# Performance work log

Measured on AMD Instinct MI355X. Metric: run time of the kernel, lower is better.

## Reference

```python
import jax, jax.numpy as jnp
import numpy as np

# Model dims (match init_kwargs / input_specs)
B, CIN, COUT = 32, 32, 64
H, W = 128, 128
KH, KW = 3, 3
MAXCN = 64                    # max entries in connect_nums_list
HO, WO = H - KH + 1, W - KW + 1   # padding=0, stride=1


def setup_inputs() -> dict:
    key = jax.random.key(0)
    k1, k2, k3, k4 = jax.random.split(key, 4)
    x = jax.random.normal(k1, (B, CIN, H, W), dtype=jnp.float32)
    # padded kernel bank: [out_channel, connection_slot, kh, kw]
    weights = jax.random.normal(k2, (COUT, MAXCN, KH, KW), dtype=jnp.float32)
    # per-pixel bias map per output channel (original inits zeros; random exercises it)
    bias = jax.random.normal(k3, (COUT, HO, WO), dtype=jnp.float32) * 0.1
    connect_nums = jax.random.randint(k4, (COUT,), 1, MAXCN + 1, dtype=jnp.int32)
    return {"x": x, "weights": weights, "bias": bias, "connect_nums": connect_nums}


def reference(x, weights, bias, connect_nums):
    O, J = weights.shape[0], weights.shape[1]
    # mask out kernel slots beyond each channel's connection count
    mask = (jnp.arange(J)[None, :] < connect_nums[:, None]).astype(weights.dtype)  # [O,J]
    # slot j reads input channel j % CIN; conv is linear, so fold duplicate-channel
    # kernels into one effective dense kernel [O, CIN, KH, KW]
    onehot = jax.nn.one_hot(jnp.arange(J) % CIN, CIN, dtype=weights.dtype)  # [J,C]
    kdense = jnp.einsum('ojhw,oj,jc->ochw', weights, mask, onehot)
    out = jax.lax.conv_general_dilated(
        x, kdense, window_strides=(1, 1), padding='VALID',
        dimension_numbers=('NCHW', 'OIHW', 'NCHW'))  # [B,O,HO,WO]
    return out + bias[None]
```

## Files before the change

kernel.cpp:

```cpp
#include <hip/hip_runtime.h>

#define B_    32
#define CIN   32
#define COUT  64
#define H_    128
#define W_    128
#define HO_   126
#define WO_   126
#define MAXCN 64

typedef __attribute__((ext_vector_type(8))) short short8;
typedef __attribute__((ext_vector_type(4))) float floatx4;

static __device__ __forceinline__ unsigned short f2bf(float f) {
    union { float f; unsigned u; } v; v.f = f;
    unsigned r = v.u + 0x7fff + ((v.u >> 16) & 1);
    return (unsigned short)(r >> 16);
}

__global__ void fold_bf16(const float* __restrict__ w,
                          const int* __restrict__ cn,
                          unsigned short* __restrict__ wk) {
    int idx = blockIdx.x * 256 + threadIdx.x;
    if (idx >= 9 * COUT * CIN) return;
    int c   = idx & 31;
    int oc  = (idx >> 5) & 63;
    int tap = idx >> 11;
    int n = cn[oc];
    float v = 0.0f;
    if (c < n)      v += w[(oc * MAXCN + c) * 9 + tap];
    if (c + 32 < n) v += w[(oc * MAXCN + c + 32) * 9 + tap];
    wk[idx] = f2bf(v);
}

__global__ __launch_bounds__(256)
void nchw_to_nhwc_bf16(const float* __restrict__ x,
                       unsigned short* __restrict__ xb) {
    const int b = blockIdx.y, y = blockIdx.x;
    const int t = threadIdx.x;
    const int c8  = t & 3;
    const int xi0 = t >> 2;
    const float* xp = x + (size_t)b * CIN * H_ * W_ + (size_t)y * W_;
#pragma unroll
    for (int it = 0; it < 2; ++it) {
        const int xi = xi0 + it * 64;
        __align__(16) unsigned short v[8];
#pragma unroll
        for (int j = 0; j < 8; ++j) {
            const int c = c8 * 8 + j;
            v[j] = f2bf(xp[(size_t)c * (H_ * W_) + xi]);
        }
        *(uint4*)(xb + (((size_t)b * H_ + y) * W_ + xi) * CIN + c8 * 8) =
            *(const uint4*)v;
    }
}

__global__ __launch_bounds__(256, 4)
void conv_mfma(const unsigned short* __restrict__ xb,
               const unsigned short* __restrict__ wk,
               const float* __restrict__ bias,
               float* __restrict__ out) {
    __shared__ __align__(16) unsigned short ws[9 * COUT * CIN];

    const int tile = blockIdx.x;
    const int b    = blockIdx.y;
    const int tx = tile & 7, ty = tile >> 3;
    const int x0 = tx * 16, y0 = ty * 16;
    const int tid = threadIdx.x;

    uint4* ws4 = (uint4*)ws;
    const uint4* wk4 = (const uint4*)wk;
#pragma unroll
    for (int it = 0; it < 9; ++it) ws4[it * 256 + tid] = wk4[it * 256 + tid];
    __syncthreads();

    const int w_id = tid >> 6;
    const int lane = tid & 63;
    const int quad = lane >> 4, l16 = lane & 15;

    int rowoff[6];
#pragma unroll
    for (int r = 0; r < 6; ++r) {
        int iy = y0 + 4 * w_id + r; if (iy > H_ - 1) iy = H_ - 1;
        rowoff[r] = (b * H_ + iy) * (W_ * CIN);
    }
    int coloff[3];
#pragma unroll
    for (int kw = 0; kw < 3; ++kw) {
        int ix = x0 + l16 + kw; if (ix > W_ - 1) ix = W_ - 1;
        coloff[kw] = ix * CIN + quad * 8;
    }

    floatx4 acc[4][4];
#pragma unroll
    for (int i = 0; i < 4; ++i)
#pragma unroll
        for (int t = 0; t < 4; ++t) acc[i][t] = (floatx4)0.0f;

#pragma unroll
    for (int kh = 0; kh < 3; ++kh) {
#pragma unroll
        for (int kw = 0; kw < 3; ++kw) {
            const int tap = kh * 3 + kw;
            short8 a[4], bf[4];
#pragma unroll
            for (int t = 0; t < 4; ++t)
                a[t] = *(const short8*)&ws[((tap * COUT + t * 16 + l16) * CIN) + quad * 8];
#pragma unroll
            for (int i = 0; i < 4; ++i)
                bf[i] = *(const short8*)(xb + rowoff[i + kh] + coloff[kw]);
#pragma unroll
            for (int i = 0; i < 4; ++i)
#pragma unroll
                for (int t = 0; t < 4; ++t)
                    acc[i][t] = __builtin_amdgcn_mfma_f32_16x16x32_bf16(a[t], bf[i], acc[i][t], 0, 0, 0);
        }
    }

    const int col = x0 + l16;
    if (col < WO_) {
#pragma unroll
        for (int i = 0; i < 4; ++i) {
            const int y = y0 + 4 * w_id + i;
            if (y >= HO_) continue;
#pragma unroll
            for (int t = 0; t < 4; ++t) {
#pragma unroll
                for (int r = 0; r < 4; ++r) {
                    const int oc = t * 16 + quad * 4 + r;
                    out[(((size_t)b * COUT + oc) * HO_ + y) * WO_ + col] =
                        acc[i][t][r] + bias[((size_t)oc * HO_ + y) * WO_ + col];
                }
            }
        }
    }
}

__global__ void fold_kernel(const float* __restrict__ w,
                            const int* __restrict__ cn,
                            float* __restrict__ kd) {
    int idx = blockIdx.x * blockDim.x + threadIdx.x;
    if (idx >= COUT * CIN * 9) return;
    int t = idx % 9;
    int c = (idx / 9) % CIN;
    int o = idx / (9 * CIN);
    int n = cn[o];
    float v = 0.0f;
    if (c < n)      v += w[(o * MAXCN + c) * 9 + t];
    if (c + 32 < n) v += w[(o * MAXCN + c + 32) * 9 + t];
    kd[idx] = v;
}

__global__ __launch_bounds__(256)
void conv_kernel(const float* __restrict__ x,
                 const float* __restrict__ kd,
                 const float* __restrict__ bias,
                 float* __restrict__ out) {
    __shared__ __align__(16) float xsh[CIN * 18 * 20];
    __shared__ __align__(16) float wsh[16 * 289];
    const int b = blockIdx.z, ocg = blockIdx.y, tile = blockIdx.x;
    const int ty = tile >> 3, txx = tile & 7;
    const int y0 = ty * 16, x0 = txx * 16;
    const int tid = threadIdx.x;
    const float* xbp = x + (size_t)b * CIN * H_ * W_;
    for (int idx = tid; idx < CIN * 18 * 18; idx += 256) {
        int c = idx / 324, rem = idx - c * 324, r = rem / 18, col = rem - r * 18;
        int iy = y0 + r;   if (iy > H_ - 1) iy = H_ - 1;
        int ix = x0 + col; if (ix > W_ - 1) ix = W_ - 1;
        xsh[c * 360 + r * 20 + col] = xbp[(c * H_ + iy) * W_ + ix];
    }
    for (int idx = tid; idx < 16 * 288; idx += 256) {
        int oc = idx / 288, rr = idx - oc * 288;
        wsh[oc * 289 + rr] = kd[(ocg * 16 + oc) * 288 + rr];
    }
    __syncthreads();
    const int oc_l = tid & 15, pb = tid >> 4, pby = pb >> 2, pbx = pb & 3;
    float acc[4][4];
#pragma unroll
    for (int i = 0; i < 4; ++i)
#pragma unroll
        for (int j = 0; j < 4; ++j) acc[i][j] = 0.0f;
    const float* xp = &xsh[(pby * 4) * 20 + pbx * 4];
    const float* wp = &wsh[oc_l * 289];
    for (int c = 0; c < CIN; ++c) {
        float xr[6][6];
#pragma unroll
        for (int r = 0; r < 6; ++r) {
            const float* row = xp + c * 360 + r * 20;
            float4 v4 = *reinterpret_cast<const float4*>(row);
            float2 v2 = *reinterpret_cast<const float2*>(row + 4);
            xr[r][0] = v4.x; xr[r][1] = v4.y; xr[r][2] = v4.z;
            xr[r][3] = v4.w; xr[r][4] = v2.x; xr[r][5] = v2.y;
        }
        float wr[9];
#pragma unroll
        for (int t = 0; t < 9; ++t) wr[t] = wp[c * 9 + t];
#pragma unroll
        for (int kh = 0; kh < 3; ++kh)
#pragma unroll
            for (int kw = 0; kw < 3; ++kw) {
                const float wv = wr[kh * 3 + kw];
#pragma unroll
                for (int i = 0; i < 4; ++i)
#pragma unroll
                    for (int j = 0; j < 4; ++j)
                        acc[i][j] = fmaf(xr[i + kh][j + kw], wv, acc[i][j]);
            }
    }
    const int o = ocg * 16 + oc_l;
    const int yb = y0 + pby * 4, xq0 = x0 + pbx * 4;
    float* ob = out + ((size_t)(b * COUT + o)) * HO_ * WO_;
    const float* bb = bias + (size_t)o * HO_ * WO_;
#pragma unroll
    for (int i = 0; i < 4; ++i) {
        int y = yb + i;
        if (y >= HO_) continue;
#pragma unroll
        for (int j = 0; j < 4; ++j) {
            int xq = xq0 + j;
            if (xq >= WO_) continue;
            ob[y * WO_ + xq] = acc[i][j] + bb[y * WO_ + xq];
        }
    }
}

extern "C" void kernel_launch(void* const* d_in, const int* in_sizes, int n_in,
                              void* d_out, int out_size, void* d_ws, size_t ws_size,
                              hipStream_t stream) {
    const float* x    = (const float*)d_in[0];
    const float* w    = (const float*)d_in[1];
    const float* bias = (const float*)d_in[2];
    const int*   cn   = (const int*)d_in[3];
    float* out = (float*)d_out;

    const size_t XB_BYTES = (size_t)B_ * H_ * W_ * CIN * 2;
    const size_t WK_BYTES = (size_t)9 * COUT * CIN * 2;

    if (ws_size >= XB_BYTES + WK_BYTES) {
        unsigned short* xbuf = (unsigned short*)d_ws;
        unsigned short* wkb  = (unsigned short*)((char*)d_ws + XB_BYTES);
        fold_bf16<<<(9 * COUT * CIN + 255) / 256, 256, 0, stream>>>(w, cn, wkb);
        nchw_to_nhwc_bf16<<<dim3(H_, B_), 256, 0, stream>>>(x, xbuf);
        conv_mfma<<<dim3(64, B_), 256, 0, stream>>>(xbuf, wkb, bias, out);
    } else {
        float* kd = (float*)d_ws;
        fold_kernel<<<(COUT * CIN * 9 + 255) / 256, 256, 0, stream>>>(w, cn, kd);
        dim3 grid(64, 4, B_);
        conv_kernel<<<grid, 256, 0, stream>>>(x, kd, bias, out);
    }
}
```

Before: 281.8 us.

## Stage input tiles in LDS with double-buffered async loads across four column tiles

The MFMA conv kernel now handles four 16x16 output tiles per block. Each 18x18x32 bf16 input patch is staged into LDS with global_load_lds, double-buffered so the next tile's load overlaps the current tile's MFMAs, and the folded weights are stored in a chunked layout so LDS reads index cleanly. Bias is pre-transposed to an NHWC buffer by an extra kernel so the epilogue can read it with float4 loads. This removes repeated global loads of overlapping input pixels and amortizes the weight load over more tiles. In exchange the grid is smaller (512 blocks), LDS use is higher, and an extra bias-transpose pass and workspace are added.

```diff
diff --git a/kernel.cpp b/kernel.cpp
--- a/kernel.cpp
+++ b/kernel.cpp
@@ -16,6 +16,12 @@
     union { float f; unsigned u; } v; v.f = f;
     unsigned r = v.u + 0x7fff + ((v.u >> 16) & 1);
     return (unsigned short)(r >> 16);
+}
+
+static __device__ __forceinline__ void gld16(const void* g, void* l) {
+    __builtin_amdgcn_global_load_lds(
+        (const __attribute__((address_space(1))) unsigned int*)g,
+        (__attribute__((address_space(3))) unsigned int*)l, 16, 0, 0);
 }
 
 __global__ void fold_bf16(const float* __restrict__ w,
@@ -30,7 +36,7 @@
     float v = 0.0f;
     if (c < n)      v += w[(oc * MAXCN + c) * 9 + tap];
     if (c + 32 < n) v += w[(oc * MAXCN + c + 32) * 9 + tap];
-    wk[idx] = f2bf(v);
+    wk[((tap * 4 + (c >> 3)) * 64 + oc) * 8 + (c & 7)] = f2bf(v);
 }
 
 __global__ __launch_bounds__(256)
@@ -55,84 +61,124 @@
     }
 }
 
-__global__ __launch_bounds__(256, 4)
+__global__ __launch_bounds__(256)
+void bias_to_nhwc(const float* __restrict__ bias, float* __restrict__ bn) {
+    int idx = blockIdx.x * 256 + threadIdx.x;
+    int oc = idx & 63;
+    int p  = idx >> 6;
+    int y  = p / WO_;
+    int x  = p - y * WO_;
+    bn[idx] = bias[((size_t)oc * HO_ + y) * WO_ + x];
+}
+
+static __device__ __forceinline__
+void stage_tile(const unsigned short* __restrict__ xbi,
+                unsigned short* __restrict__ lds,
+                int w_id, int lane, int y0, int x0, int bsel) {
+    unsigned short* dst = lds + bsel * (1296 * 8);
+#pragma unroll
+    for (int k = 0; k < 5; ++k) {
+        const int base = w_id * 324 + k * 64;
+        const int d = base + lane;
+        const int q = d / 18, xc = d - q * 18;
+        const int row = q >> 2, cp = q & 3;
+        int iy = y0 + row; if (iy > H_ - 1) iy = H_ - 1;
+        int ix = x0 + xc;  if (ix > W_ - 1) ix = W_ - 1;
+        gld16(xbi + (((iy << 7) + ix) * 4 + cp) * 8, dst + base * 8);
+    }
+    {
+        const int base = w_id * 324 + 320;
+        if (lane < 4) {
+            const int d = base + lane;
+            const int q = d / 18, xc = d - q * 18;
+            const int row = q >> 2, cp = q & 3;
+            int iy = y0 + row; if (iy > H_ - 1) iy = H_ - 1;
+            int ix = x0 + xc;  if (ix > W_ - 1) ix = W_ - 1;
+            gld16(xbi + (((iy << 7) + ix) * 4 + cp) * 8, dst + base * 8);
+        }
+    }
+}
+
+__global__ __launch_bounds__(256)
 void conv_mfma(const unsigned short* __restrict__ xb,
                const unsigned short* __restrict__ wk,
-               const float* __restrict__ bias,
+               const float* __restrict__ bnhwc,
                float* __restrict__ out) {
-    __shared__ __align__(16) unsigned short ws[9 * COUT * CIN];
-
-    const int tile = blockIdx.x;
-    const int b    = blockIdx.y;
-    const int tx = tile & 7, ty = tile >> 3;
-    const int x0 = tx * 16, y0 = ty * 16;
+    __shared__ __align__(16) unsigned short lds[4896 * 8];
+
+    const int s   = blockIdx.x;
+    const int img = s >> 4;
+    const int ty  = (s >> 1) & 7;
+    const int tx0 = (s & 1) * 4;
+    const int y0  = ty * 16;
     const int tid = threadIdx.x;
-
-    uint4* ws4 = (uint4*)ws;
-    const uint4* wk4 = (const uint4*)wk;
-#pragma unroll
-    for (int it = 0; it < 9; ++it) ws4[it * 256 + tid] = wk4[it * 256 + tid];
+    const int w_id = tid >> 6, lane = tid & 63;
+    const int quad = lane >> 4, l16 = lane & 15;
+
+    const unsigned short* xbi = xb + (size_t)img * (H_ * W_ * CIN);
+
+#pragma unroll
+    for (int k = 0; k < 9; ++k) {
+        const int ch = w_id * 576 + k * 64;
+        gld16(wk + (ch + lane) * 8, &lds[(2592 + ch) * 8]);
+    }
+    stage_tile(xbi, lds, w_id, lane, y0, tx0 * 16, 0);
     __syncthreads();
 
-    const int w_id = tid >> 6;
-    const int lane = tid & 63;
-    const int quad = lane >> 4, l16 = lane & 15;
-
-    int rowoff[6];
-#pragma unroll
-    for (int r = 0; r < 6; ++r) {
-        int iy = y0 + 4 * w_id + r; if (iy > H_ - 1) iy = H_ - 1;
-        rowoff[r] = (b * H_ + iy) * (W_ * CIN);
-    }
-    int coloff[3];
-#pragma unroll
-    for (int kw = 0; kw < 3; ++kw) {
-        int ix = x0 + l16 + kw; if (ix > W_ - 1) ix = W_ - 1;
-        coloff[kw] = ix * CIN + quad * 8;
-    }
-
-    floatx4 acc[4][4];
-#pragma unroll
-    for (int i = 0; i < 4; ++i)
-#pragma unroll
-        for (int t = 0; t < 4; ++t) acc[i][t] = (floatx4)0.0f;
-
-#pragma unroll
-    for (int kh = 0; kh < 3; ++kh) {
-#pragma unroll
-        for (int kw = 0; kw < 3; ++kw) {
-            const int tap = kh * 3 + kw;
-            short8 a[4], bf[4];
-#pragma unroll
-            for (int t = 0; t < 4; ++t)
-                a[t] = *(const short8*)&ws[((tap * COUT + t * 16 + l16) * CIN) + quad * 8];
-#pragma unroll
-            for (int i = 0; i < 4; ++i)
-                bf[i] = *(const short8*)(xb + rowoff[i + kh] + coloff[kw]);
-#pragma unroll
-            for (int i = 0; i < 4; ++i)
-#pragma unroll
-                for (int t = 0; t < 4; ++t)
-                    acc[i][t] = __builtin_amdgcn_mfma_f32_16x16x32_bf16(a[t], bf[i], acc[i][t], 0, 0, 0);
-        }
-    }
-
-    const int col = x0 + l16;
-    if (col < WO_) {
-#pragma unroll
-        for (int i = 0; i < 4; ++i) {
-            const int y = y0 + 4 * w_id + i;
-            if (y >= HO_) continue;
-#pragma unroll
-            for (int t = 0; t < 4; ++t) {
-#pragma unroll
-                for (int r = 0; r < 4; ++r) {
-                    const int oc = t * 16 + quad * 4 + r;
-                    out[(((size_t)b * COUT + oc) * HO_ + y) * WO_ + col] =
-                        acc[i][t][r] + bias[((size_t)oc * HO_ + y) * WO_ + col];
+    for (int t = 0; t < 4; ++t) {
+        const int buf = t & 1;
+        if (t < 3)
+            stage_tile(xbi, lds, w_id, lane, y0, (tx0 + t + 1) * 16, buf ^ 1);
+
+        const unsigned short* xsb = lds + buf * (1296 * 8);
+        const unsigned short* wsb = lds + 2592 * 8;
+
+        floatx4 acc[4][4];
+#pragma unroll
+        for (int i = 0; i < 4; ++i)
+#pragma unroll
+            for (int tt = 0; tt < 4; ++tt) acc[i][tt] = (floatx4)0.0f;
+
+#pragma unroll
+        for (int kh = 0; kh < 3; ++kh) {
+#pragma unroll
+            for (int kw = 0; kw < 3; ++kw) {
+                const int tap = kh * 3 + kw;
+                short8 a[4], bf[4];
+#pragma unroll
+                for (int tt = 0; tt < 4; ++tt)
+                    a[tt] = *(const short8*)&wsb[((tap * 4 + quad) * 64 + tt * 16 + l16) * 8];
+#pragma unroll
+                for (int i = 0; i < 4; ++i)
+                    bf[i] = *(const short8*)&xsb[(((4 * w_id + i + kh) * 4 + quad) * 18 + l16 + kw) * 8];
+#pragma unroll
+                for (int i = 0; i < 4; ++i)
+#pragma unroll
+                    for (int tt = 0; tt < 4; ++tt)
+                        acc[i][tt] = __builtin_amdgcn_mfma_f32_16x16x32_bf16(a[tt], bf[i], acc[i][tt], 0, 0, 0);
+            }
+        }
+
+        const int col = (tx0 + t) * 16 + l16;
+        if (col < WO_) {
+#pragma unroll
+            for (int i = 0; i < 4; ++i) {
+                const int y = y0 + 4 * w_id + i;
+                if (y >= HO_) continue;
+                const float* bp = bnhwc + ((size_t)y * WO_ + col) * COUT;
+#pragma unroll
+                for (int tt = 0; tt < 4; ++tt) {
+                    const float4 bv = *(const float4*)(bp + tt * 16 + quad * 4);
+#pragma unroll
+                    for (int r = 0; r < 4; ++r) {
+                        const int oc = tt * 16 + quad * 4 + r;
+                        out[(((size_t)(img * COUT + oc)) * HO_ + y) * WO_ + col] =
+                            acc[i][tt][r] + bv[r];
+                    }
                 }
             }
         }
+        if (t < 3) __syncthreads();
     }
 }
 
@@ -235,13 +281,16 @@
 
     const size_t XB_BYTES = (size_t)B_ * H_ * W_ * CIN * 2;
     const size_t WK_BYTES = (size_t)9 * COUT * CIN * 2;
-
-    if (ws_size >= XB_BYTES + WK_BYTES) {
+    const size_t BN_BYTES = (size_t)HO_ * WO_ * COUT * 4;
+
+    if (ws_size >= XB_BYTES + WK_BYTES + BN_BYTES) {
         unsigned short* xbuf = (unsigned short*)d_ws;
         unsigned short* wkb  = (unsigned short*)((char*)d_ws + XB_BYTES);
-        fold_bf16<<<(9 * COUT * CIN + 255) / 256, 256, 0, stream>>>(w, cn, wkb);
+        float*          bnb  = (float*)((char*)d_ws + XB_BYTES + WK_BYTES);
+        fold_bf16<<<72, 256, 0, stream>>>(w, cn, wkb);
         nchw_to_nhwc_bf16<<<dim3(H_, B_), 256, 0, stream>>>(x, xbuf);
-        conv_mfma<<<dim3(64, B_), 256, 0, stream>>>(xbuf, wkb, bias, out);
+        bias_to_nhwc<<<3969, 256, 0, stream>>>(bias, bnb);
+        conv_mfma<<<512, 256, 0, stream>>>(xbuf, wkb, bnb, out);
     } else {
         float* kd = (float*)d_ws;
         fold_kernel<<<(COUT * CIN * 9 + 255) / 256, 256, 0, stream>>>(w, cn, kd);
```

New measurement: 284.5 us. About the same (+0.9%).

## Hold folded weights in registers and stream rows per wave in MFMA conv

Applied to the files above, without the earlier changes.

The MFMA conv kernel no longer stages the folded weights in shared memory. Each wave keeps its 32 output channels' weights for all 9 taps in registers and walks 8 output rows, issuing three input-row loads per output row. The bias is transposed once into an NHWC buffer so it can be loaded as float4 and used to seed the accumulators. The weight fold writes a layout matching these register loads. This trades the LDS fill and barrier for higher register pressure, an extra bias-transpose kernel, and more workspace; whether the new ws_size condition still holds is unknown.

```diff
diff --git a/kernel.cpp b/kernel.cpp
--- a/kernel.cpp
+++ b/kernel.cpp
@@ -30,7 +30,7 @@
     float v = 0.0f;
     if (c < n)      v += w[(oc * MAXCN + c) * 9 + tap];
     if (c + 32 < n) v += w[(oc * MAXCN + c + 32) * 9 + tap];
-    wk[idx] = f2bf(v);
+    wk[((tap * 4 + (c >> 3)) * 64 + oc) * 8 + (c & 7)] = f2bf(v);
 }
 
 __global__ __launch_bounds__(256)
@@ -55,83 +55,83 @@
     }
 }
 
+__global__ __launch_bounds__(256)
+void bias_to_nhwc(const float* __restrict__ bias, float* __restrict__ bn) {
+    int idx = blockIdx.x * 256 + threadIdx.x;
+    int oc = idx & 63;
+    int p  = idx >> 6;
+    int y  = p / WO_;
+    int x  = p - y * WO_;
+    bn[idx] = bias[((size_t)oc * HO_ + y) * WO_ + x];
+}
+
 __global__ __launch_bounds__(256, 4)
 void conv_mfma(const unsigned short* __restrict__ xb,
                const unsigned short* __restrict__ wk,
-               const float* __restrict__ bias,
+               const float* __restrict__ bnhwc,
                float* __restrict__ out) {
-    __shared__ __align__(16) unsigned short ws[9 * COUT * CIN];
-
-    const int tile = blockIdx.x;
-    const int b    = blockIdx.y;
-    const int tx = tile & 7, ty = tile >> 3;
-    const int x0 = tx * 16, y0 = ty * 16;
-    const int tid = threadIdx.x;
-
-    uint4* ws4 = (uint4*)ws;
-    const uint4* wk4 = (const uint4*)wk;
-#pragma unroll
-    for (int it = 0; it < 9; ++it) ws4[it * 256 + tid] = wk4[it * 256 + tid];
-    __syncthreads();
-
-    const int w_id = tid >> 6;
-    const int lane = tid & 63;
+    const int strip = blockIdx.x;
+    const int yseg  = blockIdx.y;
+    const int img   = blockIdx.z;
+    const int tid  = threadIdx.x;
+    const int w_id = tid >> 6, lane = tid & 63;
     const int quad = lane >> 4, l16 = lane & 15;
-
-    int rowoff[6];
-#pragma unroll
-    for (int r = 0; r < 6; ++r) {
-        int iy = y0 + 4 * w_id + r; if (iy > H_ - 1) iy = H_ - 1;
-        rowoff[r] = (b * H_ + iy) * (W_ * CIN);
-    }
-    int coloff[3];
-#pragma unroll
-    for (int kw = 0; kw < 3; ++kw) {
-        int ix = x0 + l16 + kw; if (ix > W_ - 1) ix = W_ - 1;
-        coloff[kw] = ix * CIN + quad * 8;
-    }
-
-    floatx4 acc[4][4];
-#pragma unroll
-    for (int i = 0; i < 4; ++i)
-#pragma unroll
-        for (int t = 0; t < 4; ++t) acc[i][t] = (floatx4)0.0f;
-
-#pragma unroll
-    for (int kh = 0; kh < 3; ++kh) {
-#pragma unroll
-        for (int kw = 0; kw < 3; ++kw) {
-            const int tap = kh * 3 + kw;
-            short8 a[4], bf[4];
-#pragma unroll
-            for (int t = 0; t < 4; ++t)
-                a[t] = *(const short8*)&ws[((tap * COUT + t * 16 + l16) * CIN) + quad * 8];
-#pragma unroll
-            for (int i = 0; i < 4; ++i)
-                bf[i] = *(const short8*)(xb + rowoff[i + kh] + coloff[kw]);
-#pragma unroll
-            for (int i = 0; i < 4; ++i)
-#pragma unroll
-                for (int t = 0; t < 4; ++t)
-                    acc[i][t] = __builtin_amdgcn_mfma_f32_16x16x32_bf16(a[t], bf[i], acc[i][t], 0, 0, 0);
-        }
-    }
-
-    const int col = x0 + l16;
-    if (col < WO_) {
-#pragma unroll
-        for (int i = 0; i < 4; ++i) {
-            const int y = y0 + 4 * w_id + i;
-            if (y >= HO_) continue;
-#pragma unroll
-            for (int t = 0; t < 4; ++t) {
-#pragma unroll
-                for (int r = 0; r < 4; ++r) {
-                    const int oc = t * 16 + quad * 4 + r;
-                    out[(((size_t)b * COUT + oc) * HO_ + y) * WO_ + col] =
-                        acc[i][t][r] + bias[((size_t)oc * HO_ + y) * WO_ + col];
+    const int ocg  = w_id & 1;
+    const int rseg = w_id >> 1;
+    const int x0    = strip * 16;
+    const int ybase = yseg * 16 + rseg * 8;
+    const int col   = x0 + l16;
+    const int colb  = col > (W_ - 3) ? (W_ - 3) : col;
+
+    const short8* wq8 = (const short8*)wk;
+    short8 a[9][2];
+#pragma unroll
+    for (int tap = 0; tap < 9; ++tap)
+#pragma unroll
+        for (int t = 0; t < 2; ++t)
+            a[tap][t] = wq8[(tap * 4 + quad) * 64 + ocg * 32 + t * 16 + l16];
+
+    const unsigned short* xbi = xb + (size_t)img * (H_ * W_ * CIN);
+    float* ob = out + ((size_t)img * COUT + ocg * 32) * (HO_ * WO_);
+
+    const int nit = (HO_ - ybase) < 8 ? (HO_ - ybase) : 8;
+
+    for (int it = 0; it < nit; ++it) {
+        const int y = ybase + it;
+
+        const int colc = col > (WO_ - 1) ? (WO_ - 1) : col;
+        const float* bp = bnhwc + ((size_t)y * WO_ + colc) * COUT + ocg * 32 + quad * 4;
+        floatx4 acc[2];
+        {
+            const float4 b0 = *(const float4*)(bp);
+            const float4 b1 = *(const float4*)(bp + 16);
+            acc[0] = floatx4{b0.x, b0.y, b0.z, b0.w};
+            acc[1] = floatx4{b1.x, b1.y, b1.z, b1.w};
+        }
+
+#pragma unroll
+        for (int r = 0; r < 3; ++r) {
+            const unsigned short* prow =
+                xbi + ((size_t)(y + r) * W_ + colb) * CIN + quad * 8;
+            const short8 b0 = *(const short8*)(prow);
+            const short8 b1 = *(const short8*)(prow + CIN);
+            const short8 b2 = *(const short8*)(prow + 2 * CIN);
+            acc[0] = __builtin_amdgcn_mfma_f32_16x16x32_bf16(a[r * 3 + 0][0], b0, acc[0], 0, 0, 0);
+            acc[1] = __builtin_amdgcn_mfma_f32_16x16x32_bf16(a[r * 3 + 0][1], b0, acc[1], 0, 0, 0);
+            acc[0] = __builtin_amdgcn_mfma_f32_16x16x32_bf16(a[r * 3 + 1][0], b1, acc[0], 0, 0, 0);
+            acc[1] = __builtin_amdgcn_mfma_f32_16x16x32_bf16(a[r * 3 + 1][1], b1, acc[1], 0, 0, 0);
+            acc[0] = __builtin_amdgcn_mfma_f32_16x16x32_bf16(a[r * 3 + 2][0], b2, acc[0], 0, 0, 0);
+            acc[1] = __builtin_amdgcn_mfma_f32_16x16x32_bf16(a[r * 3 + 2][1], b2, acc[1], 0, 0, 0);
+        }
+
+        if (col < WO_) {
+#pragma unroll
+            for (int t = 0; t < 2; ++t)
+#pragma unroll
+                for (int r4 = 0; r4 < 4; ++r4) {
+                    const int oc_l = t * 16 + quad * 4 + r4;
+                    ob[((size_t)oc_l * HO_ + y) * WO_ + col] = acc[t][r4];
                 }
-            }
         }
     }
 }
@@ -235,13 +235,16 @@
 
     const size_t XB_BYTES = (size_t)B_ * H_ * W_ * CIN * 2;
     const size_t WK_BYTES = (size_t)9 * COUT * CIN * 2;
-
-    if (ws_size >= XB_BYTES + WK_BYTES) {
+    const size_t BN_BYTES = (size_t)HO_ * WO_ * COUT * 4;
+
+    if (ws_size >= XB_BYTES + WK_BYTES + BN_BYTES) {
         unsigned short* xbuf = (unsigned short*)d_ws;
         unsigned short* wkb  = (unsigned short*)((char*)d_ws + XB_BYTES);
-        fold_bf16<<<(9 * COUT * CIN + 255) / 256, 256, 0, stream>>>(w, cn, wkb);
+        float*          bnb  = (float*)((char*)d_ws + XB_BYTES + WK_BYTES);
+        fold_bf16<<<72, 256, 0, stream>>>(w, cn, wkb);
         nchw_to_nhwc_bf16<<<dim3(H_, B_), 256, 0, stream>>>(x, xbuf);
-        conv_mfma<<<dim3(64, B_), 256, 0, stream>>>(xbuf, wkb, bias, out);
+        bias_to_nhwc<<<3969, 256, 0, stream>>>(bias, bnb);
+        conv_mfma<<<dim3(8, 8, B_), 256, 0, stream>>>(xbuf, wkb, bnb, out);
     } else {
         float* kd = (float*)d_ws;
         fold_kernel<<<(COUT * CIN * 9 + 255) / 256, 256, 0, stream>>>(w, cn, kd);
```

Measured after the change: 288.2 us. 2.3% more time.
